# Kernel tuning notes

Measured on AMD Instinct MI355X. Metric: run time of the kernel, lower is better.

Reference implementation:

```python
import jax, jax.numpy as jnp
import numpy as np

B, T, NEMBD, NVOCAB, HID = 32, 64, 64, 256, 4096


def setup_inputs() -> dict:
    key = jax.random.key(0)
    ks = jax.random.split(key, 12)
    s = 0.1  # keep activations in a sane range
    return {
        "X": jax.random.randint(ks[0], (B, T), 0, NVOCAB, dtype=jnp.int32),
        "M": jnp.ones((B, T, 1), dtype=jnp.float32),
        "S": jnp.zeros((2, B, HID), dtype=jnp.float32),
        "embd": jax.random.normal(ks[1], (NVOCAB, NEMBD), jnp.float32) * s,
        "wx": jax.random.normal(ks[2], (NEMBD, 4 * HID), jnp.float32) * s,
        "wh": jax.random.normal(ks[3], (HID, 4 * HID), jnp.float32) * s,
        "wmx": jax.random.normal(ks[4], (NEMBD, HID), jnp.float32) * s,
        "wmh": jax.random.normal(ks[5], (HID, HID), jnp.float32) * s,
        "b": jnp.zeros((4 * HID,), jnp.float32),
        "gx": jax.random.normal(ks[6], (4 * HID,), jnp.float32),
        "gh": jax.random.normal(ks[7], (4 * HID,), jnp.float32),
        "gmx": jax.random.normal(ks[8], (HID,), jnp.float32),
        "gmh": jax.random.normal(ks[9], (HID,), jnp.float32),
        "w_out": jax.random.normal(ks[10], (HID, NVOCAB), jnp.float32) * s,
        "b_out": jnp.zeros((NVOCAB,), jnp.float32),
    }


def _wn(w, g):
    # tf.nn.l2_normalize(w, dim=0) * g  (column-wise weight norm)
    return w * (g / jnp.sqrt(jnp.sum(w * w, axis=0, keepdims=True).clip(1e-12)))


def reference(X, M, S, embd, wx, wh, wmx, wmh, b, gx, gh, gmx, gmh, w_out, b_out):
    # weight-normalized rnn weights (rnn_wn=True)
    wxn, whn = _wn(wx, gx), _wn(wh, gh)
    wmxn, wmhn = _wn(wmx, gmx), _wn(wmh, gmh)

    words = embd[X]                       # [B,T,64]
    xs = jnp.swapaxes(words, 0, 1)        # [T,B,64]
    ms = jnp.swapaxes(M, 0, 1)            # [T,B,1]
    c0, h0 = S[0], S[1]                   # [B,HID] each

    def step(carry, inp):
        c, h = carry
        x, mt = inp
        m = (x @ wmxn) * (h @ wmhn)       # multiplicative intermediate
        z = x @ wxn + m @ whn + b         # [B,4*HID]
        i, f, o, u = jnp.split(z, 4, axis=1)
        i, f, o = jax.nn.sigmoid(i), jax.nn.sigmoid(f), jax.nn.sigmoid(o)
        u = jnp.tanh(u)
        ct = f * c + i * u
        ht = o * jnp.tanh(ct)
        c = ct * mt + c * (1.0 - mt)      # mask-blend state
        h = ht * mt + h * (1.0 - mt)
        return (c, h), (c, h)

    (cf, hf), (cells, hs) = jax.lax.scan(step, (c0, h0), (xs, ms))
    states = jnp.stack([cf, hf], 0)       # [2,B,HID]
    # tf.concat(hs,1) then reshape [-1,HID] => batch-major (b, t) row order
    hflat = jnp.swapaxes(hs, 0, 1).reshape(-1, hs.shape[-1])  # [B*T,HID]
    logits = hflat @ w_out + b_out        # out_wn=False
    return cells, states, logits
```

## Files before the change

### kernel.cpp

```cpp
#include <hip/hip_runtime.h>
#include <hip/hip_bf16.h>

#define HID 4096
#define NEMBD 64
#define NBATCH 32
#define NTIME 64
#define NVOCAB 256
#define G4 16384

typedef __attribute__((ext_vector_type(4))) float f32x4;
typedef __attribute__((ext_vector_type(8))) short s16x8;

__device__ __forceinline__ unsigned short f2bf(float f) {
  union { float f; unsigned u; } v; v.f = f;
  unsigned u = v.u + 0x7FFFu + ((v.u >> 16) & 1u);
  return (unsigned short)(u >> 16);
}

__device__ __forceinline__ int apoff(int b, int j) {
  return ((j >> 5) << 10) | ((b >> 4) << 9) |
         (((b & 15) | (((j >> 3) & 3) << 4)) << 3) | (j & 7);
}

__global__ void colsum_k(const float* __restrict__ w, float* __restrict__ ss,
                         int K, int N, int KS) {
  int col = threadIdx.x & 63, kg = threadIdx.x >> 6;
  int j = blockIdx.x * 64 + col;
  int kper = K / KS;
  int k0 = blockIdx.y * kper;
  float s = 0.f;
#pragma unroll 4
  for (int k = k0 + kg; k < k0 + kper; k += 4) {
    float v = w[(size_t)k * N + j];
    s += v * v;
  }
  __shared__ float red[4][64];
  red[kg][col] = s;
  __syncthreads();
  if (threadIdx.x < 64)
    ss[(size_t)blockIdx.y * N + j] = red[0][col] + red[1][col] + red[2][col] + red[3][col];
}

__global__ void pack_k(const float* __restrict__ src, const float* __restrict__ ss,
                       const float* __restrict__ g, unsigned short* __restrict__ dst,
                       int N, int Cw, int S, int Kw, int nch, int KS) {
  int bid = blockIdx.x;
  int colbase = (bid & 3) * Cw + (bid >> S) * 16;
  int kbase = (bid & 3) * Kw;
  int cper = nch / gridDim.y;
  int c0 = blockIdx.y * cper;
  size_t dstbase = (size_t)bid * nch * 512 + (size_t)c0 * 512;
  __shared__ unsigned short tile[512];
  int tid = threadIdx.x;
  int col16 = tid & 15, kk = tid >> 4;
  float sc = 1.f;
  if (ss) {
    float t = 0.f;
    for (int q = 0; q < KS; ++q) t += ss[(size_t)q * N + colbase + col16];
    sc = g[colbase + col16] / sqrtf(fmaxf(t, 1e-12f));
  }
  for (int c = c0; c < c0 + cper; ++c) {
    for (int h = 0; h < 2; ++h) {
      int kk2 = kk + h * 16;
      int k = kbase + c * 32 + kk2;
      float v = src[(size_t)k * N + colbase + col16] * sc;
      int l = col16 | (((kk2 >> 3) & 3) << 4);
      tile[l * 8 + (kk2 & 7)] = f2bf(v);
    }
    __syncthreads();
    if (tid < 64)
      ((s16x8*)(dst + dstbase + (size_t)(c - c0) * 512))[tid] = ((s16x8*)tile)[tid];
    __syncthreads();
  }
}

__global__ void xepack_k(const int* __restrict__ X, const float* __restrict__ embd,
                         unsigned short* __restrict__ xe) {
  int t = blockIdx.x;
  int tid = threadIdx.x;
  int l = tid & 63, tile = (tid >> 6) & 1, c2 = tid >> 7;
  int b = tile * 16 + (l & 15);
  int row = X[b * NTIME + t];
  int k0 = 32 * c2 + 8 * (l >> 4);
  size_t off = (size_t)t * 2048 + c2 * 1024 + tile * 512 + l * 8;
  for (int j = 0; j < 8; ++j) xe[off + j] = f2bf(embd[row * NEMBD + k0 + j]);
}

__global__ void init_k(const float* __restrict__ S, float* __restrict__ cst,
                       float* __restrict__ hst, unsigned short* __restrict__ hpk) {
  int e = blockIdx.x * 256 + threadIdx.x;
  if (e < NBATCH * HID) {
    float c = S[e], h = S[NBATCH * HID + e];
    cst[e] = c; hst[e] = h;
    int b = e >> 12, j = e & 4095;
    hpk[apoff(b, j)] = f2bf(h);
  }
}

#define MFMA(a, b, c) __builtin_amdgcn_mfma_f32_16x16x32_bf16(a, b, c, 0, 0, 0)

__global__ __launch_bounds__(1024)
void ph1_k(const unsigned short* __restrict__ wmhp, const unsigned short* __restrict__ wmxp,
           const unsigned short* __restrict__ xe, const unsigned short* __restrict__ hpk,
           unsigned short* __restrict__ mpk, int t) {
  const int g = blockIdx.x;
  const int tid = threadIdx.x;
  const int w = tid >> 6, l = tid & 63;
  const int lo = l & 15, hi = l >> 4;

  __shared__ float part[16][32][16];
  __shared__ float xmS[32][16];

  const s16x8* wmh_g = (const s16x8*)(wmhp + (size_t)g * 128 * 512);
  const s16x8* wmx_g = (const s16x8*)(wmxp + (size_t)g * 2 * 512);
  const s16x8* hp = (const s16x8*)hpk;

  f32x4 a0 = {0.f, 0.f, 0.f, 0.f}, a1 = {0.f, 0.f, 0.f, 0.f};
#pragma unroll
  for (int q = 0; q < 8; ++q) {
    int cc = w * 8 + q;
    s16x8 bf = wmh_g[cc * 64 + l];
    a0 = MFMA(hp[cc * 128 + l], bf, a0);
    a1 = MFMA(hp[cc * 128 + 64 + l], bf, a1);
  }
#pragma unroll
  for (int r = 0; r < 4; ++r) {
    part[w][4 * hi + r][lo] = a0[r];
    part[w][16 + 4 * hi + r][lo] = a1[r];
  }
  if (w == 0) {
    f32x4 x0 = {0.f, 0.f, 0.f, 0.f}, x1 = {0.f, 0.f, 0.f, 0.f};
    const s16x8* xep = (const s16x8*)(xe + (size_t)t * 2048);
#pragma unroll
    for (int c2 = 0; c2 < 2; ++c2) {
      s16x8 bf = wmx_g[c2 * 64 + l];
      x0 = MFMA(xep[c2 * 128 + l], bf, x0);
      x1 = MFMA(xep[c2 * 128 + 64 + l], bf, x1);
    }
#pragma unroll
    for (int r = 0; r < 4; ++r) {
      xmS[4 * hi + r][lo] = x0[r];
      xmS[16 + 4 * hi + r][lo] = x1[r];
    }
  }
  __syncthreads();
  if (tid < 256) {
    const int eb = tid >> 3, c0 = (tid & 7) * 2;
    const int ej = g * 16 + c0;
    float hm0 = 0.f, hm1 = 0.f;
#pragma unroll
    for (int k = 0; k < 16; ++k) {
      hm0 += part[k][eb][c0];
      hm1 += part[k][eb][c0 + 1];
    }
    unsigned pk = (unsigned)f2bf(xmS[eb][c0] * hm0) |
                  ((unsigned)f2bf(xmS[eb][c0 + 1] * hm1) << 16);
    ((unsigned*)mpk)[apoff(eb, ej) >> 1] = pk;
  }
}

__global__ __launch_bounds__(1024)
void ph2_k(const unsigned short* __restrict__ whp, const unsigned short* __restrict__ wxp,
           const unsigned short* __restrict__ xe, const float* __restrict__ bias,
           const float* __restrict__ Mm, const unsigned short* __restrict__ mpk,
           unsigned short* __restrict__ hpk, float* __restrict__ cst,
           float* __restrict__ hst, unsigned short* __restrict__ hflat,
           float* __restrict__ out, int t) {
  const int g = blockIdx.x;
  const int tid = threadIdx.x;
  const int w = tid >> 6, l = tid & 63;
  const int lo = l & 15, hi = l >> 4;
  const int gate = w & 3, ks = w >> 2;

  __shared__ float part[16][32][16];

  const s16x8* wh_w = (const s16x8*)(whp + (size_t)(g * 4 + gate) * 128 * 512);
  const s16x8* wx_w = (const s16x8*)(wxp + (size_t)(g * 4 + gate) * 2 * 512);
  const s16x8* mp = (const s16x8*)mpk;

  f32x4 z0 = {0.f, 0.f, 0.f, 0.f}, z1 = {0.f, 0.f, 0.f, 0.f};
#pragma unroll 4
  for (int q = 0; q < 32; ++q) {
    int cc = ks * 32 + q;
    s16x8 bf = wh_w[cc * 64 + l];
    z0 = MFMA(mp[cc * 128 + l], bf, z0);
    z1 = MFMA(mp[cc * 128 + 64 + l], bf, z1);
  }
  if (ks == 0) {
    const s16x8* xep = (const s16x8*)(xe + (size_t)t * 2048);
#pragma unroll
    for (int c2 = 0; c2 < 2; ++c2) {
      s16x8 bf = wx_w[c2 * 64 + l];
      z0 = MFMA(xep[c2 * 128 + l], bf, z0);
      z1 = MFMA(xep[c2 * 128 + 64 + l], bf, z1);
    }
  }
#pragma unroll
  for (int r = 0; r < 4; ++r) {
    part[w][4 * hi + r][lo] = z0[r];
    part[w][16 + 4 * hi + r][lo] = z1[r];
  }
  __syncthreads();
  if (tid < 256) {
    const int eb = tid >> 3, c0 = (tid & 7) * 2;
    const int ej = g * 16 + c0;
    float iv0 = part[0][eb][c0] + part[4][eb][c0] + part[8][eb][c0] + part[12][eb][c0] + bias[ej];
    float iv1 = part[0][eb][c0+1] + part[4][eb][c0+1] + part[8][eb][c0+1] + part[12][eb][c0+1] + bias[ej + 1];
    float fv0 = part[1][eb][c0] + part[5][eb][c0] + part[9][eb][c0] + part[13][eb][c0] + bias[4096 + ej];
    float fv1 = part[1][eb][c0+1] + part[5][eb][c0+1] + part[9][eb][c0+1] + part[13][eb][c0+1] + bias[4096 + ej + 1];
    float ov0 = part[2][eb][c0] + part[6][eb][c0] + part[10][eb][c0] + part[14][eb][c0] + bias[8192 + ej];
    float ov1 = part[2][eb][c0+1] + part[6][eb][c0+1] + part[10][eb][c0+1] + part[14][eb][c0+1] + bias[8192 + ej + 1];
    float uv0 = part[3][eb][c0] + part[7][eb][c0] + part[11][eb][c0] + part[15][eb][c0] + bias[12288 + ej];
    float uv1 = part[3][eb][c0+1] + part[7][eb][c0+1] + part[11][eb][c0+1] + part[15][eb][c0+1] + bias[12288 + ej + 1];
    iv0 = 1.f / (1.f + __expf(-iv0)); iv1 = 1.f / (1.f + __expf(-iv1));
    fv0 = 1.f / (1.f + __expf(-fv0)); fv1 = 1.f / (1.f + __expf(-fv1));
    ov0 = 1.f / (1.f + __expf(-ov0)); ov1 = 1.f / (1.f + __expf(-ov1));
    uv0 = tanhf(uv0); uv1 = tanhf(uv1);
    size_t sj = (size_t)eb * HID + ej;
    float cp0 = cst[sj], cp1 = cst[sj + 1];
    float hp0 = hst[sj], hp1 = hst[sj + 1];
    float ct0 = fv0 * cp0 + iv0 * uv0, ct1 = fv1 * cp1 + iv1 * uv1;
    float ht0 = ov0 * tanhf(ct0), ht1 = ov1 * tanhf(ct1);
    float mt = Mm[eb * NTIME + t];
    float cn0 = ct0 * mt + cp0 * (1.f - mt), cn1 = ct1 * mt + cp1 * (1.f - mt);
    float hn0 = ht0 * mt + hp0 * (1.f - mt), hn1 = ht1 * mt + hp1 * (1.f - mt);
    cst[sj] = cn0; cst[sj + 1] = cn1;
    hst[sj] = hn0; hst[sj + 1] = hn1;
    out[((size_t)t * NBATCH + eb) * HID + ej] = cn0;
    out[((size_t)t * NBATCH + eb) * HID + ej + 1] = cn1;
    unsigned hpack = (unsigned)f2bf(hn0) | ((unsigned)f2bf(hn1) << 16);
    ((unsigned*)hflat)[(((size_t)eb * NTIME + t) * HID + ej) >> 1] = hpack;
    ((unsigned*)hpk)[apoff(eb, ej) >> 1] = hpack;
    if (t == NTIME - 1) {
      out[(size_t)NTIME * NBATCH * HID + sj] = cn0;
      out[(size_t)NTIME * NBATCH * HID + sj + 1] = cn1;
      out[(size_t)NTIME * NBATCH * HID + NBATCH * HID + sj] = hn0;
      out[(size_t)NTIME * NBATCH * HID + NBATCH * HID + sj + 1] = hn1;
    }
  }
}

__global__ __launch_bounds__(256)
void logits_k(const unsigned short* __restrict__ hflat,
              const unsigned short* __restrict__ woutp,
              const float* __restrict__ bout, float* __restrict__ out) {
  int r0 = blockIdx.x * 16;
  int tid = threadIdx.x, w = tid >> 6, l = tid & 63;
  int lo = l & 15, hi = l >> 4;
  f32x4 acc[4] = {{0.f,0.f,0.f,0.f},{0.f,0.f,0.f,0.f},{0.f,0.f,0.f,0.f},{0.f,0.f,0.f,0.f}};
  const unsigned short* arow = hflat + (size_t)(r0 + lo) * HID;
  const s16x8* wp = (const s16x8*)woutp;
#pragma unroll 2
  for (int c = 0; c < 128; ++c) {
    s16x8 af = *(const s16x8*)(arow + c * 32 + 8 * hi);
#pragma unroll
    for (int q = 0; q < 4; ++q) {
      int nt = w * 4 + q;
      acc[q] = MFMA(af, wp[(nt * 128 + c) * 64 + l], acc[q]);
    }
  }
#pragma unroll
  for (int q = 0; q < 4; ++q) {
    int nt = w * 4 + q;
    int col = nt * 16 + lo;
    float bo = bout[col];
#pragma unroll
    for (int r = 0; r < 4; ++r)
      out[(size_t)(r0 + 4 * hi + r) * NVOCAB + col] = acc[q][r] + bo;
  }
}

extern "C" void kernel_launch(void* const* d_in, const int* in_sizes, int n_in,
                              void* d_out, int out_size, void* d_ws, size_t ws_size,
                              hipStream_t stream) {
  const int*   X    = (const int*)d_in[0];
  const float* Mm   = (const float*)d_in[1];
  const float* S    = (const float*)d_in[2];
  const float* embd = (const float*)d_in[3];
  const float* wx   = (const float*)d_in[4];
  const float* wh   = (const float*)d_in[5];
  const float* wmx  = (const float*)d_in[6];
  const float* wmh  = (const float*)d_in[7];
  const float* b    = (const float*)d_in[8];
  const float* gx   = (const float*)d_in[9];
  const float* gh   = (const float*)d_in[10];
  const float* gmx  = (const float*)d_in[11];
  const float* gmh  = (const float*)d_in[12];
  const float* wout = (const float*)d_in[13];
  const float* bout = (const float*)d_in[14];
  float* out = (float*)d_out;
  char* ws = (char*)d_ws;

  size_t cur = 0;
  auto alloc = [&](size_t bytes) { size_t o = cur; cur += (bytes + 255) & ~size_t(255); return o; };
  unsigned short* WHP   = (unsigned short*)(ws + alloc((size_t)1024 * 128 * 512 * 2));
  unsigned short* WMHP  = (unsigned short*)(ws + alloc((size_t)1024 * 32 * 512 * 2));
  unsigned short* WXP   = (unsigned short*)(ws + alloc((size_t)1024 * 2 * 512 * 2));
  unsigned short* WMXP  = (unsigned short*)(ws + alloc((size_t)256 * 2 * 512 * 2));
  unsigned short* WOUTP = (unsigned short*)(ws + alloc((size_t)16 * 128 * 512 * 2));
  unsigned short* XE    = (unsigned short*)(ws + alloc((size_t)64 * 2048 * 2));
  unsigned short* MPK   = (unsigned short*)(ws + alloc((size_t)32 * 4096 * 2));
  unsigned short* HPK   = (unsigned short*)(ws + alloc((size_t)32 * 4096 * 2));
  float* CST            = (float*)(ws + alloc((size_t)32 * 4096 * 4));
  float* HST            = (float*)(ws + alloc((size_t)32 * 4096 * 4));
  unsigned short* HFLAT = (unsigned short*)(ws + alloc((size_t)2048 * 4096 * 2));
  float* SSH            = (float*)(ws + alloc((size_t)8 * 16384 * 4));
  float* SSMH           = (float*)(ws + alloc((size_t)8 * 4096 * 4));
  float* SSX            = (float*)(ws + alloc((size_t)16384 * 4));
  float* SSMX           = (float*)(ws + alloc((size_t)4096 * 4));
  (void)ws_size; (void)in_sizes; (void)n_in; (void)out_size;

  colsum_k<<<dim3(256, 8), 256, 0, stream>>>(wh,  SSH,  HID, G4,  8);
  colsum_k<<<dim3(64, 8),  256, 0, stream>>>(wmh, SSMH, HID, HID, 8);
  colsum_k<<<dim3(256, 1), 256, 0, stream>>>(wx,  SSX,  NEMBD, G4,  1);
  colsum_k<<<dim3(64, 1),  256, 0, stream>>>(wmx, SSMX, NEMBD, HID, 1);

  pack_k<<<dim3(1024, 8), 256, 0, stream>>>(wh,  SSH,  gh,  WHP,  G4,  4096, 2, 0,    128, 8);
  pack_k<<<dim3(1024, 4), 256, 0, stream>>>(wmh, SSMH, gmh, WMHP, HID, 0,    2, 1024, 32,  8);
  pack_k<<<dim3(1024, 1), 256, 0, stream>>>(wx,  SSX,  gx,  WXP,  G4,  4096, 2, 0,    2,   1);
  pack_k<<<dim3(256, 1),  256, 0, stream>>>(wmx, SSMX, gmx, WMXP, HID, 0,    0, 0,    2,   1);
  pack_k<<<dim3(16, 1),   256, 0, stream>>>(wout, nullptr, nullptr, WOUTP, NVOCAB, 0, 0, 0, 128, 0);

  xepack_k<<<64, 256, 0, stream>>>(X, embd, XE);
  init_k<<<512, 256, 0, stream>>>(S, CST, HST, HPK);

  for (int t = 0; t < NTIME; ++t) {
    ph1_k<<<256, 1024, 0, stream>>>(WMHP, WMXP, XE, HPK, MPK, t);
    ph2_k<<<256, 1024, 0, stream>>>(WHP, WXP, XE, b, Mm, MPK, HPK, CST, HST, HFLAT, out, t);
  }

  logits_k<<<128, 256, 0, stream>>>(HFLAT, WOUTP, bout,
                                    out + (size_t)NTIME * NBATCH * HID + 2 * NBATCH * HID);
}
```

Before: 2.827 ms.

## Prefetch ph2 operands, repack WMH and hflat layouts, split logits tiles

The ph2 recurrent GEMM loop now keeps a four-deep register ring of weight and activation fragments, so global loads are issued several MFMAs ahead. The WMH packing changes from a four-way K-split over 1024 blocks to 256 column blocks, each holding the full K range, which ph1 (not shown) must consume. hflat is written directly in an MFMA-fragment layout so logits_k can read its A operand with coalesced vector loads, and logits uses twice as many blocks with fewer accumulators each. The changes cost extra VGPRs for the prefetch ring, and the WMH layout change risks a mismatch with ph1's indexing.

```diff
diff --git a/kernel.cpp b/kernel.cpp
--- a/kernel.cpp
+++ b/kernel.cpp
@@ -43,10 +43,9 @@
 
 __global__ void pack_k(const float* __restrict__ src, const float* __restrict__ ss,
                        const float* __restrict__ g, unsigned short* __restrict__ dst,
-                       int N, int Cw, int S, int Kw, int nch, int KS) {
+                       int N, int Cw, int S, int nch, int KS) {
   int bid = blockIdx.x;
   int colbase = (bid & 3) * Cw + (bid >> S) * 16;
-  int kbase = (bid & 3) * Kw;
   int cper = nch / gridDim.y;
   int c0 = blockIdx.y * cper;
   size_t dstbase = (size_t)bid * nch * 512 + (size_t)c0 * 512;
@@ -62,7 +61,7 @@
   for (int c = c0; c < c0 + cper; ++c) {
     for (int h = 0; h < 2; ++h) {
       int kk2 = kk + h * 16;
-      int k = kbase + c * 32 + kk2;
+      int k = c * 32 + kk2;
       float v = src[(size_t)k * N + colbase + col16] * sc;
       int l = col16 | (((kk2 >> 3) & 3) << 4);
       tile[l * 8 + (kk2 & 7)] = f2bf(v);
@@ -159,7 +158,7 @@
   }
 }
 
-__global__ __launch_bounds__(1024)
+__global__ __launch_bounds__(1024, 4)
 void ph2_k(const unsigned short* __restrict__ whp, const unsigned short* __restrict__ wxp,
            const unsigned short* __restrict__ xe, const float* __restrict__ bias,
            const float* __restrict__ Mm, const unsigned short* __restrict__ mpk,
@@ -179,12 +178,27 @@
   const s16x8* mp = (const s16x8*)mpk;
 
   f32x4 z0 = {0.f, 0.f, 0.f, 0.f}, z1 = {0.f, 0.f, 0.f, 0.f};
-#pragma unroll 4
-  for (int q = 0; q < 32; ++q) {
-    int cc = ks * 32 + q;
-    s16x8 bf = wh_w[cc * 64 + l];
-    z0 = MFMA(mp[cc * 128 + l], bf, z0);
-    z1 = MFMA(mp[cc * 128 + 64 + l], bf, z1);
+  const int cb = ks * 32;
+  {
+    s16x8 wbuf[4], pa[4], pb[4];
+#pragma unroll
+    for (int q = 0; q < 4; ++q) {
+      wbuf[q] = wh_w[(cb + q) * 64 + l];
+      pa[q] = mp[(cb + q) * 128 + l];
+      pb[q] = mp[(cb + q) * 128 + 64 + l];
+    }
+#pragma unroll
+    for (int q = 0; q < 32; ++q) {
+      const int r = q & 3;
+      s16x8 bf = wbuf[r], af = pa[r], gf = pb[r];
+      if (q < 28) {
+        wbuf[r] = wh_w[(cb + q + 4) * 64 + l];
+        pa[r] = mp[(cb + q + 4) * 128 + l];
+        pb[r] = mp[(cb + q + 4) * 128 + 64 + l];
+      }
+      z0 = MFMA(af, bf, z0);
+      z1 = MFMA(gf, bf, z1);
+    }
   }
   if (ks == 0) {
     const s16x8* xep = (const s16x8*)(xe + (size_t)t * 2048);
@@ -229,7 +243,14 @@
     out[((size_t)t * NBATCH + eb) * HID + ej] = cn0;
     out[((size_t)t * NBATCH + eb) * HID + ej + 1] = cn1;
     unsigned hpack = (unsigned)f2bf(hn0) | ((unsigned)f2bf(hn1) << 16);
-    ((unsigned*)hflat)[(((size_t)eb * NTIME + t) * HID + ej) >> 1] = hpack;
+    {
+      int tle = eb * 4 + (t >> 4);
+      int r16 = t & 15;
+      int kk2 = ej & 31;
+      int lane2 = r16 | (((kk2 >> 3) & 3) << 4);
+      size_t hoff = (size_t)tle * 65536 + (size_t)(ej >> 5) * 512 + lane2 * 8 + (kk2 & 7);
+      ((unsigned*)hflat)[hoff >> 1] = hpack;
+    }
     ((unsigned*)hpk)[apoff(eb, ej) >> 1] = hpack;
     if (t == NTIME - 1) {
       out[(size_t)NTIME * NBATCH * HID + sj] = cn0;
@@ -241,28 +262,26 @@
 }
 
 __global__ __launch_bounds__(256)
-void logits_k(const unsigned short* __restrict__ hflat,
+void logits_k(const unsigned short* __restrict__ hpA,
               const unsigned short* __restrict__ woutp,
               const float* __restrict__ bout, float* __restrict__ out) {
-  int r0 = blockIdx.x * 16;
+  int tle = blockIdx.x >> 1, ch = blockIdx.x & 1;
   int tid = threadIdx.x, w = tid >> 6, l = tid & 63;
   int lo = l & 15, hi = l >> 4;
-  f32x4 acc[4] = {{0.f,0.f,0.f,0.f},{0.f,0.f,0.f,0.f},{0.f,0.f,0.f,0.f},{0.f,0.f,0.f,0.f}};
-  const unsigned short* arow = hflat + (size_t)(r0 + lo) * HID;
+  const s16x8* ap = (const s16x8*)(hpA + (size_t)tle * 65536);
   const s16x8* wp = (const s16x8*)woutp;
-#pragma unroll 2
+  f32x4 acc[2] = {{0.f,0.f,0.f,0.f},{0.f,0.f,0.f,0.f}};
+  const int nt0 = ch * 8 + w * 2;
+#pragma unroll 4
   for (int c = 0; c < 128; ++c) {
-    s16x8 af = *(const s16x8*)(arow + c * 32 + 8 * hi);
-#pragma unroll
-    for (int q = 0; q < 4; ++q) {
-      int nt = w * 4 + q;
-      acc[q] = MFMA(af, wp[(nt * 128 + c) * 64 + l], acc[q]);
-    }
-  }
-#pragma unroll
-  for (int q = 0; q < 4; ++q) {
-    int nt = w * 4 + q;
-    int col = nt * 16 + lo;
+    s16x8 af = ap[c * 64 + l];
+    acc[0] = MFMA(af, wp[((nt0 + 0) * 128 + c) * 64 + l], acc[0]);
+    acc[1] = MFMA(af, wp[((nt0 + 1) * 128 + c) * 64 + l], acc[1]);
+  }
+  int r0 = tle * 16;
+#pragma unroll
+  for (int q = 0; q < 2; ++q) {
+    int col = (nt0 + q) * 16 + lo;
     float bo = bout[col];
 #pragma unroll
     for (int r = 0; r < 4; ++r)
@@ -294,7 +313,7 @@
   size_t cur = 0;
   auto alloc = [&](size_t bytes) { size_t o = cur; cur += (bytes + 255) & ~size_t(255); return o; };
   unsigned short* WHP   = (unsigned short*)(ws + alloc((size_t)1024 * 128 * 512 * 2));
-  unsigned short* WMHP  = (unsigned short*)(ws + alloc((size_t)1024 * 32 * 512 * 2));
+  unsigned short* WMHP  = (unsigned short*)(ws + alloc((size_t)256 * 128 * 512 * 2));
   unsigned short* WXP   = (unsigned short*)(ws + alloc((size_t)1024 * 2 * 512 * 2));
   unsigned short* WMXP  = (unsigned short*)(ws + alloc((size_t)256 * 2 * 512 * 2));
   unsigned short* WOUTP = (unsigned short*)(ws + alloc((size_t)16 * 128 * 512 * 2));
@@ -315,11 +334,11 @@
   colsum_k<<<dim3(256, 1), 256, 0, stream>>>(wx,  SSX,  NEMBD, G4,  1);
   colsum_k<<<dim3(64, 1),  256, 0, stream>>>(wmx, SSMX, NEMBD, HID, 1);
 
-  pack_k<<<dim3(1024, 8), 256, 0, stream>>>(wh,  SSH,  gh,  WHP,  G4,  4096, 2, 0,    128, 8);
-  pack_k<<<dim3(1024, 4), 256, 0, stream>>>(wmh, SSMH, gmh, WMHP, HID, 0,    2, 1024, 32,  8);
-  pack_k<<<dim3(1024, 1), 256, 0, stream>>>(wx,  SSX,  gx,  WXP,  G4,  4096, 2, 0,    2,   1);
-  pack_k<<<dim3(256, 1),  256, 0, stream>>>(wmx, SSMX, gmx, WMXP, HID, 0,    0, 0,    2,   1);
-  pack_k<<<dim3(16, 1),   256, 0, stream>>>(wout, nullptr, nullptr, WOUTP, NVOCAB, 0, 0, 0, 128, 0);
+  pack_k<<<dim3(1024, 8), 256, 0, stream>>>(wh,  SSH,  gh,  WHP,  G4,  4096, 2, 128, 8);
+  pack_k<<<dim3(256, 4),  256, 0, stream>>>(wmh, SSMH, gmh, WMHP, HID, 0,    0, 128, 8);
+  pack_k<<<dim3(1024, 1), 256, 0, stream>>>(wx,  SSX,  gx,  WXP,  G4,  4096, 2, 2,   1);
+  pack_k<<<dim3(256, 1),  256, 0, stream>>>(wmx, SSMX, gmx, WMXP, HID, 0,    0, 2,   1);
+  pack_k<<<dim3(16, 1),   256, 0, stream>>>(wout, nullptr, nullptr, WOUTP, NVOCAB, 0, 0, 128, 0);
 
   xepack_k<<<64, 256, 0, stream>>>(X, embd, XE);
   init_k<<<512, 256, 0, stream>>>(S, CST, HST, HPK);
@@ -329,6 +348,6 @@
     ph2_k<<<256, 1024, 0, stream>>>(WHP, WXP, XE, b, Mm, MPK, HPK, CST, HST, HFLAT, out, t);
   }
 
-  logits_k<<<128, 256, 0, stream>>>(HFLAT, WOUTP, bout,
+  logits_k<<<256, 256, 0, stream>>>(HFLAT, WOUTP, bout,
                                     out + (size_t)NTIME * NBATCH * HID + 2 * NBATCH * HID);
 }
```

Measured after the change: 2.430 ms. -14.1%, faster.
